# Kernel tuning notes

Hardware: AMD Instinct MI355X
Metric: run time of the kernel (lower is better)

The kernel has to match this reference:

```python
import jax, jax.numpy as jnp
import numpy as np

N = 1048576   # collocation points
K = 8         # number of subdomains / subnets
H = 64        # hidden width
PI = float(np.pi)


def setup_inputs() -> dict:
    key = jax.random.key(0)
    ks = jax.random.split(key, 10)
    x = jax.random.normal(ks[0], (N, 1), jnp.float32)
    t = jax.random.uniform(ks[1], (N, 1), dtype=jnp.float32)

    def xav(k, shape, fan_in, fan_out):
        # xavier_normal_ std = sqrt(2/(fan_in+fan_out))
        return jax.random.normal(k, shape, jnp.float32) * np.sqrt(2.0 / (fan_in + fan_out))

    W1 = xav(ks[2], (K, H, 3), 3, H)
    W2 = xav(ks[3], (K, H, H), H, H)
    W3 = xav(ks[4], (K, H, H), H, H)
    W4 = xav(ks[5], (K, H, H), H, H)
    W5 = xav(ks[6], (K, 1, H), H, 1)
    b1 = jnp.zeros((K, H), jnp.float32)
    b2 = jnp.zeros((K, H), jnp.float32)
    b3 = jnp.zeros((K, H), jnp.float32)
    b4 = jnp.zeros((K, H), jnp.float32)
    b5 = jnp.zeros((K, 1), jnp.float32)
    scales = jnp.full((K, 4), 5.0, jnp.float32)          # ScaledTanh scale per layer per subnet
    centers = jax.random.normal(ks[7], (K, 2), jnp.float32) * 0.5  # (mu_x, mu_t)
    log_gammas = jnp.full((K, 2), 3.0, jnp.float32)
    return dict(x=x, t=t, W1=W1, b1=b1, W2=W2, b2=b2, W3=W3, b3=b3,
                W4=W4, b4=b4, W5=W5, b5=b5, scales=scales,
                centers=centers, log_gammas=log_gammas)


def reference(x, t, W1, b1, W2, b2, W3, b3, W4, b4, W5, b5, scales, centers, log_gammas):
    # Periodic embedding: [N,2]
    x_emb = jnp.concatenate([jnp.cos(PI * x), jnp.sin(PI * x)], axis=1)
    xt = jnp.concatenate([x, t], axis=1)           # [N,2]
    inp = jnp.concatenate([x_emb, t], axis=1)      # [N,3]

    # Gaussian-window logits and softmax gating over subnets
    gamma = jnp.exp(log_gammas)                    # [K,2]
    diff_sq = (xt[:, None, :] - centers[None, :, :]) ** 2  # [N,K,2]
    logits = -jnp.sum(gamma[None, :, :] * diff_sq, axis=-1)  # [N,K]
    w = jax.nn.softmax(logits, axis=1)             # [N,K]

    u_out = jnp.zeros_like(x)                      # [N,1]
    for i in range(K):  # small fixed set of structurally-distinct subnets
        h = jnp.tanh(scales[i, 0] * (inp @ W1[i].T + b1[i]))
        h = jnp.tanh(scales[i, 1] * (h @ W2[i].T + b2[i]))
        h = jnp.tanh(scales[i, 2] * (h @ W3[i].T + b3[i]))
        h = jnp.tanh(scales[i, 3] * (h @ W4[i].T + b4[i]))
        o = h @ W5[i].T + b5[i]                    # [N,1]
        u_out = u_out + w[:, i:i + 1] * o

    u0 = x ** 2 * jnp.cos(PI * x)
    return jnp.tanh(t) * u_out + u0
```

## Files before the change

kernel.cpp:

```cpp
#include <hip/hip_runtime.h>
#include <hip/hip_bf16.h>
#include <stdint.h>

typedef __attribute__((ext_vector_type(8)))  short    s16x8;
typedef __attribute__((ext_vector_type(16))) float    f32x16;
typedef __attribute__((ext_vector_type(4)))  float    f32x4;
typedef __attribute__((ext_vector_type(4)))  unsigned u32x4;

#define KSUB 8
#define SUBSZ  27648
#define OFF_W  0
#define OFF_W1 24576
#define OFF_W5 26624
#define OFF_B  26752

#define WS_CNT (SUBSZ * KSUB)
#define WS_BKT (WS_CNT + 512)

#define LOG2E 1.4426950408889634f
#define TWOLOG2E 2.885390081777927f
#define TAU 1e-3f

__device__ __forceinline__ float fast_tanh(float z) {
  float e = __builtin_amdgcn_exp2f(z * TWOLOG2E);
  return __builtin_fmaf(-2.0f, __builtin_amdgcn_rcpf(e + 1.0f), 1.0f);
}
__device__ __forceinline__ float tanh_pre(float zeta) {
  float e = __builtin_amdgcn_exp2f(zeta);
  return __builtin_fmaf(-2.0f, __builtin_amdgcn_rcpf(e + 1.0f), 1.0f);
}
__device__ __forceinline__ unsigned packbf(float lo, float hi) {
  unsigned ul = __builtin_bit_cast(unsigned, lo) + 0x8000u;
  unsigned uh = __builtin_bit_cast(unsigned, hi) + 0x8000u;
  return __builtin_amdgcn_perm(uh, ul, 0x07060302u);
}
__device__ __forceinline__ f32x16 mfma_bf16(s16x8 a, s16x8 b, f32x16 c) {
  return __builtin_amdgcn_mfma_f32_32x32x16_bf16(a, b, c, 0, 0, 0);
}

__device__ __forceinline__ void epilogue(const f32x16& acc0, const f32x16& acc1,
                                         unsigned Bu[16]) {
#pragma unroll
  for (int kt = 0; kt < 4; ++kt) {
#pragma unroll
    for (int qq = 0; qq < 2; ++qq) {
      const int ra = ((2 * kt) & 3) * 4 + 2 * qq;
      const int rb = ((2 * kt + 1) & 3) * 4 + 2 * qq;
      float a0v, a1v, b0v, b1v;
      if (kt < 2) { a0v = acc0[ra]; a1v = acc0[ra + 1]; b0v = acc0[rb]; b1v = acc0[rb + 1]; }
      else        { a0v = acc1[ra]; a1v = acc1[ra + 1]; b0v = acc1[rb]; b1v = acc1[rb + 1]; }
      unsigned P0 = packbf(tanh_pre(a0v), tanh_pre(a1v));
      unsigned P1 = packbf(tanh_pre(b0v), tanh_pre(b1v));
      auto pr = __builtin_amdgcn_permlane32_swap(P0, P1, false, false);
      Bu[kt * 4 + qq]     = pr[0];
      Bu[kt * 4 + qq + 2] = pr[1];
    }
  }
}

__global__ void prep_weights(const float* __restrict__ W1, const float* __restrict__ b1,
                             const float* __restrict__ W2, const float* __restrict__ b2,
                             const float* __restrict__ W3, const float* __restrict__ b3,
                             const float* __restrict__ W4, const float* __restrict__ b4,
                             const float* __restrict__ W5, const float* __restrict__ scales,
                             char* __restrict__ ws) {
  const int sub = blockIdx.x;
  const int tid = threadIdx.x;
  char* dst = ws + sub * SUBSZ;
  const float s0 = TWOLOG2E * scales[sub * 4 + 0];
  const float s1 = TWOLOG2E * scales[sub * 4 + 1];
  const float s2 = TWOLOG2E * scales[sub * 4 + 2];
  const float s3 = TWOLOG2E * scales[sub * 4 + 3];
#pragma unroll
  for (int l = 0; l < 3; ++l) {
    const float* src = (l == 0) ? (W2 + sub * 4096) : (l == 1) ? (W3 + sub * 4096) : (W4 + sub * 4096);
    const float sc   = (l == 0) ? s1 : (l == 1) ? s2 : s3;
    __hip_bfloat16* d = (__hip_bfloat16*)(dst + OFF_W + l * 8192);
    for (int idx = tid; idx < 4096; idx += 256) {
      int row = idx >> 6, col = idx & 63;
      int de = row * 64 + (col ^ ((row & 7) << 3));
      d[de] = __float2bfloat16(sc * src[idx]);
    }
  }
  {
    __hip_bfloat16* d = (__hip_bfloat16*)(dst + OFF_W1);
    for (int idx = tid; idx < 1024; idx += 256) {
      int row = idx >> 4, kc = idx & 15;
      float v = 0.f;
      if (kc < 3)       v = s0 * W1[sub * 192 + row * 3 + kc];
      else if (kc == 3) v = s0 * b1[sub * 64 + row];
      d[idx] = __float2bfloat16(v);
    }
  }
  if (tid < 64) {
    ((__hip_bfloat16*)(dst + OFF_W5))[tid] = __float2bfloat16(W5[sub * 64 + tid]);
    ((float*)(dst + OFF_B))[tid]        = s1 * b2[sub * 64 + tid];
    ((float*)(dst + OFF_B + 256))[tid]  = s2 * b3[sub * 64 + tid];
    ((float*)(dst + OFF_B + 512))[tid]  = s3 * b4[sub * 64 + tid];
  }
}

#define GCHUNK 8
__global__ __launch_bounds__(256) void gate_bucket(
    const float* __restrict__ X, const float* __restrict__ T,
    const float* __restrict__ centers, const float* __restrict__ lgam,
    unsigned* __restrict__ counts, unsigned* __restrict__ buckets, int n) {
  __shared__ unsigned tot[8], cursor[8];
  const int tid  = threadIdx.x;
  const int lane = tid & 63;
  const int base = blockIdx.x * (256 * GCHUNK);
  if (tid < 8) tot[tid] = 0;
  __syncthreads();

  for (int c = 0; c < GCHUNK; ++c) {
    const int p = base + c * 256 + tid;
    const float x = X[p], tt = T[p];
    float lgv[8]; float m = -1e30f;
#pragma unroll
    for (int i = 0; i < 8; ++i) {
      float gx = __builtin_amdgcn_exp2f(lgam[2 * i] * LOG2E);
      float gt = __builtin_amdgcn_exp2f(lgam[2 * i + 1] * LOG2E);
      float dx = x - centers[2 * i], dt = tt - centers[2 * i + 1];
      float lg = -(gx * dx * dx + gt * dt * dt);
      lgv[i] = lg; m = fmaxf(m, lg);
    }
    float S = 0.f; float ev[8];
#pragma unroll
    for (int i = 0; i < 8; ++i) { ev[i] = __builtin_amdgcn_exp2f((lgv[i] - m) * LOG2E); S += ev[i]; }
    const float thr = TAU * S;
#pragma unroll
    for (int i = 0; i < 8; ++i) {
      unsigned long long b = __ballot(ev[i] > thr);
      if (lane == 0) atomicAdd(&tot[i], (unsigned)__popcll(b));
    }
  }
  __syncthreads();
  if (tid < 8) cursor[tid] = atomicAdd(&counts[tid * 16], tot[tid]);
  __syncthreads();

  for (int c = 0; c < GCHUNK; ++c) {
    const int p = base + c * 256 + tid;
    const float x = X[p], tt = T[p];
    float lgv[8]; float m = -1e30f;
#pragma unroll
    for (int i = 0; i < 8; ++i) {
      float gx = __builtin_amdgcn_exp2f(lgam[2 * i] * LOG2E);
      float gt = __builtin_amdgcn_exp2f(lgam[2 * i + 1] * LOG2E);
      float dx = x - centers[2 * i], dt = tt - centers[2 * i + 1];
      float lg = -(gx * dx * dx + gt * dt * dt);
      lgv[i] = lg; m = fmaxf(m, lg);
    }
    float S = 0.f; float ev[8];
#pragma unroll
    for (int i = 0; i < 8; ++i) { ev[i] = __builtin_amdgcn_exp2f((lgv[i] - m) * LOG2E); S += ev[i]; }
    const float thr = TAU * S;
    const float rS = __builtin_amdgcn_rcpf(S);
#pragma unroll
    for (int i = 0; i < 8; ++i) {
      unsigned long long b = __ballot(ev[i] > thr);
      unsigned cw = (unsigned)__popcll(b);
      unsigned wb = 0;
      if (lane == 0 && cw) wb = atomicAdd(&cursor[i], cw);
      wb = __shfl(wb, 0);
      if (ev[i] > thr) {
        unsigned pre = __builtin_amdgcn_mbcnt_hi((unsigned)(b >> 32),
                        __builtin_amdgcn_mbcnt_lo((unsigned)b, 0u));
        unsigned wq = (unsigned)(ev[i] * rS * 4095.f + 0.5f);
        buckets[(size_t)i * n + wb + pre] = (wq << 20) | (unsigned)p;
      }
    }
  }
}

__global__ __launch_bounds__(256) void pinn_eval(
    const float* __restrict__ X, const float* __restrict__ T,
    const char* __restrict__ ws, const float* __restrict__ b5,
    const unsigned* __restrict__ counts, const unsigned* __restrict__ buckets,
    float* __restrict__ out, int n) {
  const int sub = blockIdx.y;
  const unsigned cnt = counts[sub * 16];
  if (blockIdx.x * 128u >= cnt) return;

  __shared__ __align__(16) char smem[SUBSZ];
  const int tid  = threadIdx.x;
  const int lane = tid & 63;
  const int wid  = tid >> 6;
  const int g    = lane >> 5;
  const int lpt  = lane & 31;

  const char* gb = ws + sub * SUBSZ;
  for (int ch = wid; ch < SUBSZ / 1024; ch += 4) {
    *(f32x4*)(smem + ch * 1024 + lane * 16) = *(const f32x4*)(gb + ch * 1024 + lane * 16);
  }

  const unsigned j = blockIdx.x * 128u + wid * 32u + (unsigned)lpt;
  const bool valid = j < cnt;
  const unsigned jj = valid ? j : (cnt - 1);
  const unsigned ent = buckets[(size_t)sub * n + jj];
  const unsigned pidx = ent & 0xFFFFFu;
  const float wsub = (float)(ent >> 20) * (1.0f / 4095.0f);
  const float x  = X[pidx];
  const float tt = T[pidx];

  float rr = x * 0.5f;
  rr = rr - floorf(rr);
  const float cpx = __builtin_amdgcn_cosf(rr);
  const float spx = __builtin_amdgcn_sinf(rr);
  unsigned b00 = packbf(cpx, spx);
  unsigned b01 = packbf(tt, 1.0f);
  if (g) { b00 = 0u; b01 = 0u; }

  __syncthreads();

  f32x16 acc0, acc1;
#pragma unroll
  for (int r = 0; r < 16; ++r) { acc0[r] = 0.f; acc1[r] = 0.f; }
  s16x8 a0 = *(const s16x8*)(smem + OFF_W1 + lpt * 32 + g * 16);
  s16x8 a1 = *(const s16x8*)(smem + OFF_W1 + (32 + lpt) * 32 + g * 16);
  u32x4 blv; blv[0] = b00; blv[1] = b01; blv[2] = 0u; blv[3] = 0u;
  s16x8 bl1 = __builtin_bit_cast(s16x8, blv);
  acc0 = mfma_bf16(a0, bl1, acc0);
  acc1 = mfma_bf16(a1, bl1, acc1);
  unsigned Bu[16];
  epilogue(acc0, acc1, Bu);

  for (int l = 0; l < 3; ++l) {
    const float* bias = (const float*)(smem + OFF_B + l * 256);
#pragma unroll
    for (int rq = 0; rq < 4; ++rq) {
      f32x4 bv0 = *(const f32x4*)(bias + 8 * rq + 4 * g);
      f32x4 bv1 = *(const f32x4*)(bias + 32 + 8 * rq + 4 * g);
#pragma unroll
      for (int rr2 = 0; rr2 < 4; ++rr2) { acc0[4 * rq + rr2] = bv0[rr2]; acc1[4 * rq + rr2] = bv1[rr2]; }
    }
    const char* wbase = smem + OFF_W + l * 8192;
#pragma unroll
    for (int kt = 0; kt < 4; ++kt) {
      const int coff = ((16 * kt + 8 * g) * 2) ^ ((lpt & 7) << 4);
      s16x8 wa0 = *(const s16x8*)(wbase + lpt * 128 + coff);
      s16x8 wa1 = *(const s16x8*)(wbase + (32 + lpt) * 128 + coff);
      u32x4 bb; bb[0] = Bu[kt * 4]; bb[1] = Bu[kt * 4 + 1]; bb[2] = Bu[kt * 4 + 2]; bb[3] = Bu[kt * 4 + 3];
      s16x8 bf = __builtin_bit_cast(s16x8, bb);
      acc0 = mfma_bf16(wa0, bf, acc0);
      acc1 = mfma_bf16(wa1, bf, acc1);
    }
    epilogue(acc0, acc1, Bu);
  }

  const float b5s = b5[sub];
  f32x16 acc5;
#pragma unroll
  for (int r = 0; r < 16; ++r) acc5[r] = b5s;
#pragma unroll
  for (int kt = 0; kt < 4; ++kt) {
    s16x8 w5f = *(const s16x8*)(smem + OFF_W5 + (kt * 16 + 8 * g) * 2);
    u32x4 bb; bb[0] = Bu[kt * 4]; bb[1] = Bu[kt * 4 + 1]; bb[2] = Bu[kt * 4 + 2]; bb[3] = Bu[kt * 4 + 3];
    s16x8 bf = __builtin_bit_cast(s16x8, bb);
    acc5 = mfma_bf16(w5f, bf, acc5);
  }

  if ((lane < 32) && valid) atomicAdd(&out[pidx], wsub * acc5[0]);
}

__global__ __launch_bounds__(256) void finalize(
    const float* __restrict__ X, const float* __restrict__ T,
    float* __restrict__ out) {
  const int p = blockIdx.x * 256 + threadIdx.x;
  const float x  = X[p];
  const float tt = T[p];
  float rr = x * 0.5f;
  rr = rr - floorf(rr);
  const float cpx = __builtin_amdgcn_cosf(rr);
  const float u0  = x * x * cpx;
  out[p] = fast_tanh(tt) * out[p] + u0;
}

__global__ __launch_bounds__(256) void pinn_main(
    const float* __restrict__ X, const float* __restrict__ T,
    const char* __restrict__ ws, const float* __restrict__ centers,
    const float* __restrict__ lgam, const float* __restrict__ b5,
    float* __restrict__ out) {
  __shared__ __align__(16) char smem[SUBSZ];
  const int tid  = threadIdx.x;
  const int lane = tid & 63;
  const int wid  = tid >> 6;
  const int g    = lane >> 5;
  const int lpt  = lane & 31;
  const int p    = blockIdx.x * 128 + wid * 32 + lpt;

  const float x  = X[p];
  const float tt = T[p];
  float rr = x * 0.5f;
  rr = rr - floorf(rr);
  const float cpx = __builtin_amdgcn_cosf(rr);
  const float spx = __builtin_amdgcn_sinf(rr);
  const float u0  = x * x * cpx;
  const float thT = fast_tanh(tt);

  float m = -1e30f;
#pragma unroll
  for (int i = 0; i < 8; ++i) {
    float gx = __builtin_amdgcn_exp2f(lgam[2 * i] * LOG2E);
    float gt = __builtin_amdgcn_exp2f(lgam[2 * i + 1] * LOG2E);
    float dx = x - centers[2 * i], dt = tt - centers[2 * i + 1];
    float lg = -(gx * dx * dx + gt * dt * dt);
    m = fmaxf(m, lg);
  }

  unsigned b00 = packbf(cpx, spx);
  unsigned b01 = packbf(tt, 1.0f);
  if (g) { b00 = 0u; b01 = 0u; }

  float uacc = 0.f, S = 0.f;

  for (int sub = 0; sub < KSUB; ++sub) {
    __syncthreads();
    const char* gb = ws + sub * SUBSZ;
    for (int ch = wid; ch < SUBSZ / 1024; ch += 4) {
      *(f32x4*)(smem + ch * 1024 + lane * 16) = *(const f32x4*)(gb + ch * 1024 + lane * 16);
    }
    __syncthreads();

    float gx = __builtin_amdgcn_exp2f(lgam[2 * sub] * LOG2E);
    float gt = __builtin_amdgcn_exp2f(lgam[2 * sub + 1] * LOG2E);
    float dx = x - centers[2 * sub], dtt = tt - centers[2 * sub + 1];
    float lg = -(gx * dx * dx + gt * dtt * dtt);
    float ei = __builtin_amdgcn_exp2f((lg - m) * LOG2E);

    f32x16 acc0, acc1;
#pragma unroll
    for (int r = 0; r < 16; ++r) { acc0[r] = 0.f; acc1[r] = 0.f; }
    s16x8 a0 = *(const s16x8*)(smem + OFF_W1 + lpt * 32 + g * 16);
    s16x8 a1 = *(const s16x8*)(smem + OFF_W1 + (32 + lpt) * 32 + g * 16);
    u32x4 blv; blv[0] = b00; blv[1] = b01; blv[2] = 0u; blv[3] = 0u;
    s16x8 bl1 = __builtin_bit_cast(s16x8, blv);
    acc0 = mfma_bf16(a0, bl1, acc0);
    acc1 = mfma_bf16(a1, bl1, acc1);
    unsigned Bu[16];
    epilogue(acc0, acc1, Bu);

    for (int l = 0; l < 3; ++l) {
      const float* bias = (const float*)(smem + OFF_B + l * 256);
#pragma unroll
      for (int rq = 0; rq < 4; ++rq) {
        f32x4 bv0 = *(const f32x4*)(bias + 8 * rq + 4 * g);
        f32x4 bv1 = *(const f32x4*)(bias + 32 + 8 * rq + 4 * g);
#pragma unroll
        for (int rr2 = 0; rr2 < 4; ++rr2) { acc0[4 * rq + rr2] = bv0[rr2]; acc1[4 * rq + rr2] = bv1[rr2]; }
      }
      const char* wbase = smem + OFF_W + l * 8192;
#pragma unroll
      for (int kt = 0; kt < 4; ++kt) {
        const int coff = ((16 * kt + 8 * g) * 2) ^ ((lpt & 7) << 4);
        s16x8 wa0 = *(const s16x8*)(wbase + lpt * 128 + coff);
        s16x8 wa1 = *(const s16x8*)(wbase + (32 + lpt) * 128 + coff);
        u32x4 bb; bb[0] = Bu[kt * 4]; bb[1] = Bu[kt * 4 + 1]; bb[2] = Bu[kt * 4 + 2]; bb[3] = Bu[kt * 4 + 3];
        s16x8 bf = __builtin_bit_cast(s16x8, bb);
        acc0 = mfma_bf16(wa0, bf, acc0);
        acc1 = mfma_bf16(wa1, bf, acc1);
      }
      epilogue(acc0, acc1, Bu);
    }

    const float b5s = b5[sub];
    f32x16 acc5;
#pragma unroll
    for (int r = 0; r < 16; ++r) acc5[r] = b5s;
#pragma unroll
    for (int kt = 0; kt < 4; ++kt) {
      s16x8 w5f = *(const s16x8*)(smem + OFF_W5 + (kt * 16 + 8 * g) * 2);
      u32x4 bb; bb[0] = Bu[kt * 4]; bb[1] = Bu[kt * 4 + 1]; bb[2] = Bu[kt * 4 + 2]; bb[3] = Bu[kt * 4 + 3];
      s16x8 bf = __builtin_bit_cast(s16x8, bb);
      acc5 = mfma_bf16(w5f, bf, acc5);
    }
    uacc = __builtin_fmaf(ei, acc5[0], uacc);
    S += ei;
  }

  float u = uacc * __builtin_amdgcn_rcpf(S);
  if (lane < 32) out[p] = thT * u + u0;
}

extern "C" void kernel_launch(void* const* d_in, const int* in_sizes, int n_in,
                              void* d_out, int out_size, void* d_ws, size_t ws_size,
                              hipStream_t stream) {
  const float* X   = (const float*)d_in[0];
  const float* T   = (const float*)d_in[1];
  const float* W1  = (const float*)d_in[2];
  const float* b1  = (const float*)d_in[3];
  const float* W2  = (const float*)d_in[4];
  const float* b2  = (const float*)d_in[5];
  const float* W3  = (const float*)d_in[6];
  const float* b3  = (const float*)d_in[7];
  const float* W4  = (const float*)d_in[8];
  const float* b4  = (const float*)d_in[9];
  const float* W5  = (const float*)d_in[10];
  const float* b5  = (const float*)d_in[11];
  const float* sc  = (const float*)d_in[12];
  const float* cen = (const float*)d_in[13];
  const float* lg  = (const float*)d_in[14];
  float* out = (float*)d_out;
  char*  ws  = (char*)d_ws;
  const int n = in_sizes[0];

  prep_weights<<<KSUB, 256, 0, stream>>>(W1, b1, W2, b2, W3, b3, W4, b4, W5, sc, ws);

  const size_t need = (size_t)WS_BKT + (size_t)KSUB * (size_t)n * 4ull;
  if (ws_size >= need) {
    unsigned* counts  = (unsigned*)(ws + WS_CNT);
    unsigned* buckets = (unsigned*)(ws + WS_BKT);
    hipMemsetAsync(counts, 0, 512, stream);
    hipMemsetAsync(out, 0, (size_t)n * 4, stream);
    gate_bucket<<<n / (256 * GCHUNK), 256, 0, stream>>>(X, T, cen, lg, counts, buckets, n);
    pinn_eval<<<dim3(n / 128, KSUB), 256, 0, stream>>>(X, T, ws, b5, counts, buckets, out, n);
    finalize<<<n / 256, 256, 0, stream>>>(X, T, out);
  } else {
    pinn_main<<<n / 128, 256, 0, stream>>>(X, T, ws, cen, lg, b5, out);
  }
}
```

Before: 282.4 us.

## Use persistent compacted tile scheduling for bucketed subnet evaluation and drop memsets

Replaces the sparse 2D grid (n/128 x 8 blocks, most exiting early) with a fixed grid of 2048 blocks. Each block walks a contiguous range of compacted tiles, located through a prefix table of per-subnet tile counts built by a tiny single-thread kernel. Weights are reloaded into shared memory only when the subnet changes. The two memsets are folded into prep_weights and gate_bucket, which removes launch and empty-block overhead at the cost of an extra small kernel and a serial loop per block.

```diff
diff --git a/kernel.cpp b/kernel.cpp
--- a/kernel.cpp
+++ b/kernel.cpp
@@ -15,7 +15,8 @@
 #define OFF_B  26752
 
 #define WS_CNT (SUBSZ * KSUB)
-#define WS_BKT (WS_CNT + 512)
+#define WS_TE  (WS_CNT + 512)
+#define WS_BKT (WS_CNT + 1024)
 
 #define LOG2E 1.4426950408889634f
 #define TWOLOG2E 2.885390081777927f
@@ -66,6 +67,7 @@
                              char* __restrict__ ws) {
   const int sub = blockIdx.x;
   const int tid = threadIdx.x;
+  if (sub == 0 && tid < 128) ((unsigned*)(ws + WS_CNT))[tid] = 0;
   char* dst = ws + sub * SUBSZ;
   const float s0 = TWOLOG2E * scales[sub * 4 + 0];
   const float s1 = TWOLOG2E * scales[sub * 4 + 1];
@@ -104,7 +106,8 @@
 __global__ __launch_bounds__(256) void gate_bucket(
     const float* __restrict__ X, const float* __restrict__ T,
     const float* __restrict__ centers, const float* __restrict__ lgam,
-    unsigned* __restrict__ counts, unsigned* __restrict__ buckets, int n) {
+    unsigned* __restrict__ counts, unsigned* __restrict__ buckets,
+    float* __restrict__ out, int n) {
   __shared__ unsigned tot[8], cursor[8];
   const int tid  = threadIdx.x;
   const int lane = tid & 63;
@@ -115,6 +118,7 @@
   for (int c = 0; c < GCHUNK; ++c) {
     const int p = base + c * 256 + tid;
     const float x = X[p], tt = T[p];
+    out[p] = 0.f;
     float lgv[8]; float m = -1e30f;
 #pragma unroll
     for (int i = 0; i < 8; ++i) {
@@ -172,94 +176,120 @@
   }
 }
 
+__global__ void make_tiles(const unsigned* __restrict__ counts, unsigned* __restrict__ te) {
+  if (threadIdx.x == 0) {
+    unsigned acc = 0;
+#pragma unroll
+    for (int i = 0; i < 8; ++i) { te[i] = acc; acc += (counts[i * 16] + 127u) >> 7; }
+    te[8] = acc;
+  }
+}
+
+#define EVG 2048
 __global__ __launch_bounds__(256) void pinn_eval(
     const float* __restrict__ X, const float* __restrict__ T,
     const char* __restrict__ ws, const float* __restrict__ b5,
     const unsigned* __restrict__ counts, const unsigned* __restrict__ buckets,
-    float* __restrict__ out, int n) {
-  const int sub = blockIdx.y;
-  const unsigned cnt = counts[sub * 16];
-  if (blockIdx.x * 128u >= cnt) return;
-
+    const unsigned* __restrict__ te, float* __restrict__ out, int n) {
   __shared__ __align__(16) char smem[SUBSZ];
+  __shared__ unsigned ste[9];
   const int tid  = threadIdx.x;
   const int lane = tid & 63;
   const int wid  = tid >> 6;
   const int g    = lane >> 5;
   const int lpt  = lane & 31;
 
-  const char* gb = ws + sub * SUBSZ;
-  for (int ch = wid; ch < SUBSZ / 1024; ch += 4) {
-    *(f32x4*)(smem + ch * 1024 + lane * 16) = *(const f32x4*)(gb + ch * 1024 + lane * 16);
-  }
-
-  const unsigned j = blockIdx.x * 128u + wid * 32u + (unsigned)lpt;
-  const bool valid = j < cnt;
-  const unsigned jj = valid ? j : (cnt - 1);
-  const unsigned ent = buckets[(size_t)sub * n + jj];
-  const unsigned pidx = ent & 0xFFFFFu;
-  const float wsub = (float)(ent >> 20) * (1.0f / 4095.0f);
-  const float x  = X[pidx];
-  const float tt = T[pidx];
-
-  float rr = x * 0.5f;
-  rr = rr - floorf(rr);
-  const float cpx = __builtin_amdgcn_cosf(rr);
-  const float spx = __builtin_amdgcn_sinf(rr);
-  unsigned b00 = packbf(cpx, spx);
-  unsigned b01 = packbf(tt, 1.0f);
-  if (g) { b00 = 0u; b01 = 0u; }
-
+  if (tid < 9) ste[tid] = te[tid];
   __syncthreads();
-
-  f32x16 acc0, acc1;
-#pragma unroll
-  for (int r = 0; r < 16; ++r) { acc0[r] = 0.f; acc1[r] = 0.f; }
-  s16x8 a0 = *(const s16x8*)(smem + OFF_W1 + lpt * 32 + g * 16);
-  s16x8 a1 = *(const s16x8*)(smem + OFF_W1 + (32 + lpt) * 32 + g * 16);
-  u32x4 blv; blv[0] = b00; blv[1] = b01; blv[2] = 0u; blv[3] = 0u;
-  s16x8 bl1 = __builtin_bit_cast(s16x8, blv);
-  acc0 = mfma_bf16(a0, bl1, acc0);
-  acc1 = mfma_bf16(a1, bl1, acc1);
-  unsigned Bu[16];
-  epilogue(acc0, acc1, Bu);
-
-  for (int l = 0; l < 3; ++l) {
-    const float* bias = (const float*)(smem + OFF_B + l * 256);
-#pragma unroll
-    for (int rq = 0; rq < 4; ++rq) {
-      f32x4 bv0 = *(const f32x4*)(bias + 8 * rq + 4 * g);
-      f32x4 bv1 = *(const f32x4*)(bias + 32 + 8 * rq + 4 * g);
-#pragma unroll
-      for (int rr2 = 0; rr2 < 4; ++rr2) { acc0[4 * rq + rr2] = bv0[rr2]; acc1[4 * rq + rr2] = bv1[rr2]; }
-    }
-    const char* wbase = smem + OFF_W + l * 8192;
+  const unsigned total = ste[8];
+  const unsigned tpb = (total + EVG - 1) / EVG;
+  const unsigned t0 = blockIdx.x * tpb;
+  const unsigned t1 = (t0 + tpb < total) ? (t0 + tpb) : total;
+  if (t0 >= total) return;
+
+  int cur_sub = -1;
+  for (unsigned tile = t0; tile < t1; ++tile) {
+    int sub = 0;
+    while (ste[sub + 1] <= tile) ++sub;
+    const unsigned cnt   = counts[sub * 16];
+    const unsigned ltile = tile - ste[sub];
+
+    if (sub != cur_sub) {
+      __syncthreads();
+      const char* gb = ws + sub * SUBSZ;
+      for (int ch = wid; ch < SUBSZ / 1024; ch += 4) {
+        *(f32x4*)(smem + ch * 1024 + lane * 16) = *(const f32x4*)(gb + ch * 1024 + lane * 16);
+      }
+      cur_sub = sub;
+      __syncthreads();
+    }
+
+    const unsigned j = ltile * 128u + wid * 32u + (unsigned)lpt;
+    const bool valid = j < cnt;
+    const unsigned jj = valid ? j : (cnt - 1);
+    const unsigned ent = buckets[(size_t)sub * n + jj];
+    const unsigned pidx = ent & 0xFFFFFu;
+    const float wsub = (float)(ent >> 20) * (1.0f / 4095.0f);
+    const float x  = X[pidx];
+    const float tt = T[pidx];
+
+    float rr = x * 0.5f;
+    rr = rr - floorf(rr);
+    const float cpx = __builtin_amdgcn_cosf(rr);
+    const float spx = __builtin_amdgcn_sinf(rr);
+    unsigned b00 = packbf(cpx, spx);
+    unsigned b01 = packbf(tt, 1.0f);
+    if (g) { b00 = 0u; b01 = 0u; }
+
+    f32x16 acc0, acc1;
+#pragma unroll
+    for (int r = 0; r < 16; ++r) { acc0[r] = 0.f; acc1[r] = 0.f; }
+    s16x8 a0 = *(const s16x8*)(smem + OFF_W1 + lpt * 32 + g * 16);
+    s16x8 a1 = *(const s16x8*)(smem + OFF_W1 + (32 + lpt) * 32 + g * 16);
+    u32x4 blv; blv[0] = b00; blv[1] = b01; blv[2] = 0u; blv[3] = 0u;
+    s16x8 bl1 = __builtin_bit_cast(s16x8, blv);
+    acc0 = mfma_bf16(a0, bl1, acc0);
+    acc1 = mfma_bf16(a1, bl1, acc1);
+    unsigned Bu[16];
+    epilogue(acc0, acc1, Bu);
+
+    for (int l = 0; l < 3; ++l) {
+      const float* bias = (const float*)(smem + OFF_B + l * 256);
+#pragma unroll
+      for (int rq = 0; rq < 4; ++rq) {
+        f32x4 bv0 = *(const f32x4*)(bias + 8 * rq + 4 * g);
+        f32x4 bv1 = *(const f32x4*)(bias + 32 + 8 * rq + 4 * g);
+#pragma unroll
+        for (int rr2 = 0; rr2 < 4; ++rr2) { acc0[4 * rq + rr2] = bv0[rr2]; acc1[4 * rq + rr2] = bv1[rr2]; }
+      }
+      const char* wbase = smem + OFF_W + l * 8192;
+#pragma unroll
+      for (int kt = 0; kt < 4; ++kt) {
+        const int coff = ((16 * kt + 8 * g) * 2) ^ ((lpt & 7) << 4);
+        s16x8 wa0 = *(const s16x8*)(wbase + lpt * 128 + coff);
+        s16x8 wa1 = *(const s16x8*)(wbase + (32 + lpt) * 128 + coff);
+        u32x4 bb; bb[0] = Bu[kt * 4]; bb[1] = Bu[kt * 4 + 1]; bb[2] = Bu[kt * 4 + 2]; bb[3] = Bu[kt * 4 + 3];
+        s16x8 bf = __builtin_bit_cast(s16x8, bb);
+        acc0 = mfma_bf16(wa0, bf, acc0);
+        acc1 = mfma_bf16(wa1, bf, acc1);
+      }
+      epilogue(acc0, acc1, Bu);
+    }
+
+    const float b5s = b5[sub];
+    f32x16 acc5;
+#pragma unroll
+    for (int r = 0; r < 16; ++r) acc5[r] = b5s;
 #pragma unroll
     for (int kt = 0; kt < 4; ++kt) {
-      const int coff = ((16 * kt + 8 * g) * 2) ^ ((lpt & 7) << 4);
-      s16x8 wa0 = *(const s16x8*)(wbase + lpt * 128 + coff);
-      s16x8 wa1 = *(const s16x8*)(wbase + (32 + lpt) * 128 + coff);
+      s16x8 w5f = *(const s16x8*)(smem + OFF_W5 + (kt * 16 + 8 * g) * 2);
       u32x4 bb; bb[0] = Bu[kt * 4]; bb[1] = Bu[kt * 4 + 1]; bb[2] = Bu[kt * 4 + 2]; bb[3] = Bu[kt * 4 + 3];
       s16x8 bf = __builtin_bit_cast(s16x8, bb);
-      acc0 = mfma_bf16(wa0, bf, acc0);
-      acc1 = mfma_bf16(wa1, bf, acc1);
-    }
-    epilogue(acc0, acc1, Bu);
-  }
-
-  const float b5s = b5[sub];
-  f32x16 acc5;
-#pragma unroll
-  for (int r = 0; r < 16; ++r) acc5[r] = b5s;
-#pragma unroll
-  for (int kt = 0; kt < 4; ++kt) {
-    s16x8 w5f = *(const s16x8*)(smem + OFF_W5 + (kt * 16 + 8 * g) * 2);
-    u32x4 bb; bb[0] = Bu[kt * 4]; bb[1] = Bu[kt * 4 + 1]; bb[2] = Bu[kt * 4 + 2]; bb[3] = Bu[kt * 4 + 3];
-    s16x8 bf = __builtin_bit_cast(s16x8, bb);
-    acc5 = mfma_bf16(w5f, bf, acc5);
-  }
-
-  if ((lane < 32) && valid) atomicAdd(&out[pidx], wsub * acc5[0]);
+      acc5 = mfma_bf16(w5f, bf, acc5);
+    }
+
+    if ((lane < 32) && valid) atomicAdd(&out[pidx], wsub * acc5[0]);
+  }
 }
 
 __global__ __launch_bounds__(256) void finalize(
@@ -408,11 +438,11 @@
   const size_t need = (size_t)WS_BKT + (size_t)KSUB * (size_t)n * 4ull;
   if (ws_size >= need) {
     unsigned* counts  = (unsigned*)(ws + WS_CNT);
+    unsigned* te      = (unsigned*)(ws + WS_TE);
     unsigned* buckets = (unsigned*)(ws + WS_BKT);
-    hipMemsetAsync(counts, 0, 512, stream);
-    hipMemsetAsync(out, 0, (size_t)n * 4, stream);
-    gate_bucket<<<n / (256 * GCHUNK), 256, 0, stream>>>(X, T, cen, lg, counts, buckets, n);
-    pinn_eval<<<dim3(n / 128, KSUB), 256, 0, stream>>>(X, T, ws, b5, counts, buckets, out, n);
+    gate_bucket<<<n / (256 * GCHUNK), 256, 0, stream>>>(X, T, cen, lg, counts, buckets, out, n);
+    make_tiles<<<1, 64, 0, stream>>>(counts, te);
+    pinn_eval<<<EVG, 256, 0, stream>>>(X, T, ws, b5, counts, buckets, te, out, n);
     finalize<<<n / 256, 256, 0, stream>>>(X, T, out);
   } else {
     pinn_main<<<n / 128, 256, 0, stream>>>(X, T, ws, cen, lg, b5, out);
```

Measured after the change: 292.5 us. 3.6% more time.
